# Optimization experiments

Measured on AMD Instinct MI355X. Metric: run time of the kernel, lower is better.

The kernel has to match this reference:

```python
import jax, jax.numpy as jnp
import numpy as np

N = 50000
E = 800000
D = 64  # d_s


def _mlp2(x, w1, b1, w2, b2):
    # Linear -> SiLU -> Linear
    return jax.nn.silu(x @ w1 + b1) @ w2 + b2


def setup_inputs() -> dict:
    key = jax.random.key(0)
    ks = jax.random.split(key, 20)
    s = jax.random.normal(ks[0], (N, D), jnp.float32)
    v = jax.random.normal(ks[1], (N, 3), jnp.float32)
    edge_index = jax.random.randint(ks[2], (2, E), 0, N, jnp.int32)
    edge_attr = jax.random.normal(ks[3], (E, D), jnp.float32)
    ev = jax.random.normal(ks[4], (E, 3), jnp.float32)
    edge_vec_unit = ev / jnp.linalg.norm(ev, axis=-1, keepdims=True)

    def lin(k, fan_in, fan_out):
        kw, kb = jax.random.split(k)
        lim = 1.0 / np.sqrt(fan_in)
        w = jax.random.uniform(kw, (fan_in, fan_out), jnp.float32, -lim, lim)
        b = jax.random.uniform(kb, (fan_out,), jnp.float32, -lim, lim)
        return w, b

    ng_w1, ng_b1 = lin(ks[5], D + 1, D)
    ng_w2, ng_b2 = lin(ks[6], D, D)
    eg_w1, eg_b1 = lin(ks[7], D + 1, D)
    eg_w2, eg_b2 = lin(ks[8], D, D)
    mg_w1, mg_b1 = lin(ks[9], 3 * D, 2 * D)
    mg_w2, mg_b2 = lin(ks[10], 2 * D, D)
    pe_w, pe_b = lin(ks[11], D, 1)
    up_w, up_b = lin(ks[12], D, D)
    ln_g = jnp.ones((D,), jnp.float32)
    ln_b = jnp.zeros((D,), jnp.float32)
    return dict(s=s, v=v, edge_index=edge_index, edge_attr=edge_attr,
                edge_vec_unit=edge_vec_unit,
                ng_w1=ng_w1, ng_b1=ng_b1, ng_w2=ng_w2, ng_b2=ng_b2,
                eg_w1=eg_w1, eg_b1=eg_b1, eg_w2=eg_w2, eg_b2=eg_b2,
                mg_w1=mg_w1, mg_b1=mg_b1, mg_w2=mg_w2, mg_b2=mg_b2,
                pe_w=pe_w, pe_b=pe_b, up_w=up_w, up_b=up_b,
                ln_g=ln_g, ln_b=ln_b)


def reference(s, v, edge_index, edge_attr, edge_vec_unit,
              ng_w1, ng_b1, ng_w2, ng_b2,
              eg_w1, eg_b1, eg_w2, eg_b2,
              mg_w1, mg_b1, mg_w2, mg_b2,
              pe_w, pe_b, up_w, up_b, ln_g, ln_b):
    row, col = edge_index[0], edge_index[1]
    s_i, s_j = s[row], s[col]            # (E, D)
    v_i, v_j = v[row], v[col]            # (E, 3)

    dot_ij = jnp.sum(v_i * edge_vec_unit, axis=-1, keepdims=True)
    dot_ji = jnp.sum(v_j * -edge_vec_unit, axis=-1, keepdims=True)
    res_ij = 1.0 - dot_ij
    res_ji = 1.0 - dot_ji
    cross_mag = jnp.linalg.norm(jnp.cross(v_i, v_j), axis=-1, keepdims=True)

    node_feat_i = _mlp2(jnp.concatenate([s_i, res_ij], -1), ng_w1, ng_b1, ng_w2, ng_b2)
    node_feat_j = _mlp2(jnp.concatenate([s_j, res_ji], -1), ng_w1, ng_b1, ng_w2, ng_b2)
    edge_feat = _mlp2(jnp.concatenate([edge_attr, cross_mag], -1), eg_w1, eg_b1, eg_w2, eg_b2)

    msg = _mlp2(jnp.concatenate([node_feat_i, node_feat_j, edge_feat], -1),
                mg_w1, mg_b1, mg_w2, mg_b2)   # (E, D)
    coeff = msg @ pe_w + pe_b                 # (E, 1)
    v_msg = edge_vec_unit * coeff             # (E, 3)

    n = s.shape[0]
    s_agg = jax.ops.segment_sum(msg, row, num_segments=n)    # (N, D)
    v_agg = jax.ops.segment_sum(v_msg, row, num_segments=n)  # (N, 3)

    s_new = s + jax.nn.silu(s_agg) @ up_w + up_b
    mu = jnp.mean(s_new, axis=-1, keepdims=True)
    var = jnp.var(s_new, axis=-1, keepdims=True)
    s_out = (s_new - mu) * jax.lax.rsqrt(var + 1e-5) * ln_g + ln_b

    v_new = v + v_agg
    denom = jnp.maximum(jnp.linalg.norm(v_new, axis=-1, keepdims=True), 1e-6)
    v_out = v_new / denom
    return (s_out, v_out)
```

## Files before the change

### kernel.cpp

```cpp
#include <hip/hip_runtime.h>
#include <math.h>

#define NN 50000
#define NE 800000
#define D 64

typedef __attribute__((ext_vector_type(8))) short short8;
typedef __attribute__((ext_vector_type(4))) float f32x4;

__device__ __forceinline__ float silu_f(float x) { return x / (1.0f + __expf(-x)); }
__device__ __forceinline__ unsigned short f2bf(float f) {
  unsigned int u = __float_as_uint(f);
  u += 0x7fffu + ((u >> 16) & 1u);
  return (unsigned short)(u >> 16);
}
__device__ __forceinline__ unsigned int pack2(float a, float b) {
  return (unsigned int)f2bf(a) | ((unsigned int)f2bf(b) << 16);
}
__device__ __forceinline__ short8 pack_frag(f32x4 a, f32x4 b) {
  union { unsigned int u[4]; short8 s; } r;
  r.u[0] = pack2(a[0], a[1]);
  r.u[1] = pack2(a[2], a[3]);
  r.u[2] = pack2(b[0], b[1]);
  r.u[3] = pack2(b[2], b[3]);
  return r.s;
}

__global__ void prep_all(const float* __restrict__ ng_w2,
                         const float* __restrict__ eg_w1,
                         const float* __restrict__ eg_w2,
                         const float* __restrict__ mg_w1,
                         const float* __restrict__ mg_w2,
                         const float* __restrict__ ng_w1,
                         const float* __restrict__ up_w,
                         unsigned short* __restrict__ out) {
  int t = blockIdx.x * 256 + threadIdx.x;
  if (t >= 104 * 64) return;
  int frag = t >> 6, L = t & 63;
  const float* W; int K, N, f0;
  if (frag < 8)       { W = ng_w2; K = 64;  N = 64;  f0 = 0; }
  else if (frag < 16) { W = eg_w1; K = 64;  N = 64;  f0 = 8; }
  else if (frag < 24) { W = eg_w2; K = 64;  N = 64;  f0 = 16; }
  else if (frag < 72) { W = mg_w1; K = 192; N = 128; f0 = 24; }
  else if (frag < 88) { W = mg_w2; K = 128; N = 64;  f0 = 72; }
  else if (frag < 96) { W = ng_w1; K = 64;  N = 64;  f0 = 88; }
  else                { W = up_w;  K = 64;  N = 64;  f0 = 96; }
  int lf = frag - f0;
  int kd = K >> 5;
  int nt = lf / kd, ks = lf % kd;
  int kb = ks * 32 + (L >> 4) * 8;
  int nc = nt * 16 + (L & 15);
  unsigned int p[4];
#pragma unroll
  for (int jj = 0; jj < 4; ++jj) {
    float a = W[(size_t)(kb + 2 * jj) * N + nc];
    float b = W[(size_t)(kb + 2 * jj + 1) * N + nc];
    p[jj] = pack2(a, b);
  }
  *(uint4*)(out + (size_t)frag * 512 + L * 8) = make_uint4(p[0], p[1], p[2], p[3]);
}

__global__ __launch_bounds__(256, 4) void node_pre(
    const float* __restrict__ s, const float* __restrict__ ng_b1,
    const unsigned short* __restrict__ WF, float* __restrict__ h_ng) {
  __shared__ __align__(16) char sm[4 * 8704];
  int tid = threadIdx.x, w = tid >> 6, lane = tid & 63;
  int l15 = lane & 15, q = lane >> 4, fb = q * 8;
  char* my = sm + w * 8704;
  int nb = (blockIdx.x * 4 + w) * 32;
  if (nb >= NN) return;

  short8 Bs[2][2];
#pragma unroll
  for (int h = 0; h < 2; ++h)
#pragma unroll
    for (int kt = 0; kt < 2; ++kt) {
      int n = nb + h * 16 + l15; if (n >= NN) n = NN - 1;
      f32x4 x0 = *(const f32x4*)(s + (size_t)n * D + kt * 32 + fb);
      f32x4 x1 = *(const f32x4*)(s + (size_t)n * D + kt * 32 + fb + 4);
      Bs[h][kt] = pack_frag(x0, x1);
    }
  short8 F[4][2]; f32x4 bb[4];
#pragma unroll
  for (int mt = 0; mt < 4; ++mt) {
    F[mt][0] = *(const short8*)(WF + (size_t)(88 + mt * 2 + 0) * 512 + lane * 8);
    F[mt][1] = *(const short8*)(WF + (size_t)(88 + mt * 2 + 1) * 512 + lane * 8);
    bb[mt] = *(const f32x4*)(ng_b1 + mt * 16 + 4 * q);
  }
#pragma unroll
  for (int h = 0; h < 2; ++h)
#pragma unroll
    for (int mt = 0; mt < 4; ++mt) {
      f32x4 acc = {0.f, 0.f, 0.f, 0.f};
      acc = __builtin_amdgcn_mfma_f32_16x16x32_bf16(F[mt][0], Bs[h][0], acc, 0, 0, 0);
      acc = __builtin_amdgcn_mfma_f32_16x16x32_bf16(F[mt][1], Bs[h][1], acc, 0, 0, 0);
      acc[0] += bb[mt][0]; acc[1] += bb[mt][1]; acc[2] += bb[mt][2]; acc[3] += bb[mt][3];
      *(f32x4*)(my + (((h * 16 + l15) * 68 + mt * 16 + 4 * q) << 2)) = acc;
    }
#pragma unroll
  for (int h = 0; h < 2; ++h)
#pragma unroll
    for (int e = 0; e < 16; ++e) {
      int n = nb + h * 16 + e;
      if (n < NN) {
        float val = *(const float*)(my + (((h * 16 + e) * 68 + lane) << 2));
        h_ng[(size_t)n * D + lane] = val;
      }
    }
}

#define LSTR 104
#define LDSW (32 * LSTR * 4)

__global__ __launch_bounds__(256, 3) void edge_mfma(
    const float* __restrict__ v, const int* __restrict__ ei,
    const float* __restrict__ edge_attr, const float* __restrict__ evu,
    const float* __restrict__ ng_w1, const float* __restrict__ ng_b2,
    const float* __restrict__ eg_w1, const float* __restrict__ eg_b1,
    const float* __restrict__ eg_b2,
    const float* __restrict__ mg_b1, const float* __restrict__ mg_b2,
    const float* __restrict__ pe_w, const float* __restrict__ pe_b,
    const float* __restrict__ h_ng,
    const unsigned short* __restrict__ WF,
    float* __restrict__ s_agg, float* __restrict__ v_agg) {
  __shared__ __align__(16) char sm[4 * LDSW];
  int tid = threadIdx.x, w = tid >> 6, lane = tid & 63;
  int l15 = lane & 15, q = lane >> 4, fb = q * 8;
  char* my = sm + w * LDSW;
  int eb = (blockIdx.x * 4 + w) * 32;

  int rown[2], coln[2];
  float rij[2], rji[2], uu0[2], uu1[2], uu2[2], cmag[2];
#pragma unroll
  for (int h = 0; h < 2; ++h) {
    int e = eb + h * 16 + l15;
    int r = ei[e], c = ei[NE + e];
    rown[h] = r; coln[h] = c;
    float u0 = evu[e * 3 + 0], u1 = evu[e * 3 + 1], u2 = evu[e * 3 + 2];
    uu0[h] = u0; uu1[h] = u1; uu2[h] = u2;
    float vi0 = v[r * 3 + 0], vi1 = v[r * 3 + 1], vi2 = v[r * 3 + 2];
    float vj0 = v[c * 3 + 0], vj1 = v[c * 3 + 1], vj2 = v[c * 3 + 2];
    rij[h] = 1.f - (vi0 * u0 + vi1 * u1 + vi2 * u2);
    rji[h] = 1.f + (vj0 * u0 + vj1 * u1 + vj2 * u2);
    float cx = vi1 * vj2 - vi2 * vj1;
    float cy = vi2 * vj0 - vi0 * vj2;
    float cz = vi0 * vj1 - vi1 * vj0;
    cmag[h] = sqrtf(cx * cx + cy * cy + cz * cz);
  }

  short8 Bai[2][2], Baj[2][2], Bxe[2][2];
  f32x4 w1l[2][2];
#pragma unroll
  for (int kt = 0; kt < 2; ++kt) {
    w1l[kt][0] = *(const f32x4*)(ng_w1 + 64 * 64 + kt * 32 + fb);
    w1l[kt][1] = *(const f32x4*)(ng_w1 + 64 * 64 + kt * 32 + fb + 4);
  }
#pragma unroll
  for (int h = 0; h < 2; ++h)
#pragma unroll
    for (int kt = 0; kt < 2; ++kt) {
      const float* pr = h_ng + (size_t)rown[h] * D + kt * 32 + fb;
      const float* pc = h_ng + (size_t)coln[h] * D + kt * 32 + fb;
      const float* px = edge_attr + (size_t)(eb + h * 16 + l15) * D + kt * 32 + fb;
      f32x4 a0 = *(const f32x4*)pr, a1 = *(const f32x4*)(pr + 4);
      f32x4 b0 = *(const f32x4*)pc, b1 = *(const f32x4*)(pc + 4);
      f32x4 x0 = *(const f32x4*)px, x1 = *(const f32x4*)(px + 4);
      f32x4 si0, si1, sj0, sj1;
#pragma unroll
      for (int c2 = 0; c2 < 4; ++c2) {
        si0[c2] = silu_f(a0[c2] + rij[h] * w1l[kt][0][c2]);
        si1[c2] = silu_f(a1[c2] + rij[h] * w1l[kt][1][c2]);
        sj0[c2] = silu_f(b0[c2] + rji[h] * w1l[kt][0][c2]);
        sj1[c2] = silu_f(b1[c2] + rji[h] * w1l[kt][1][c2]);
      }
      Bai[h][kt] = pack_frag(si0, si1);
      Baj[h][kt] = pack_frag(sj0, sj1);
      Bxe[h][kt] = pack_frag(x0, x1);
    }

  {
    short8 F[4][2]; f32x4 bb[4];
#pragma unroll
    for (int mt = 0; mt < 4; ++mt) {
      F[mt][0] = *(const short8*)(WF + (size_t)(0 + mt * 2 + 0) * 512 + lane * 8);
      F[mt][1] = *(const short8*)(WF + (size_t)(0 + mt * 2 + 1) * 512 + lane * 8);
      bb[mt] = *(const f32x4*)(ng_b2 + mt * 16 + 4 * q);
    }
#pragma unroll
    for (int h = 0; h < 2; ++h)
#pragma unroll
      for (int mt = 0; mt < 4; ++mt) {
        f32x4 ai = {0.f, 0.f, 0.f, 0.f}, aj = {0.f, 0.f, 0.f, 0.f};
        ai = __builtin_amdgcn_mfma_f32_16x16x32_bf16(F[mt][0], Bai[h][0], ai, 0, 0, 0);
        ai = __builtin_amdgcn_mfma_f32_16x16x32_bf16(F[mt][1], Bai[h][1], ai, 0, 0, 0);
        aj = __builtin_amdgcn_mfma_f32_16x16x32_bf16(F[mt][0], Baj[h][0], aj, 0, 0, 0);
        aj = __builtin_amdgcn_mfma_f32_16x16x32_bf16(F[mt][1], Baj[h][1], aj, 0, 0, 0);
        uint2 pi, pj;
        pi.x = pack2(ai[0] + bb[mt][0], ai[1] + bb[mt][1]);
        pi.y = pack2(ai[2] + bb[mt][2], ai[3] + bb[mt][3]);
        pj.x = pack2(aj[0] + bb[mt][0], aj[1] + bb[mt][1]);
        pj.y = pack2(aj[2] + bb[mt][2], aj[3] + bb[mt][3]);
        int row = h * 16 + l15;
        *(uint2*)(my + ((row * LSTR + mt * 8 + 2 * q) << 2)) = pi;
        *(uint2*)(my + ((row * LSTR + 32 + mt * 8 + 2 * q) << 2)) = pj;
      }
  }

  {
    short8 F[4][2]; f32x4 bb[4], el[4];
#pragma unroll
    for (int mt = 0; mt < 4; ++mt) {
      F[mt][0] = *(const short8*)(WF + (size_t)(8 + mt * 2 + 0) * 512 + lane * 8);
      F[mt][1] = *(const short8*)(WF + (size_t)(8 + mt * 2 + 1) * 512 + lane * 8);
      bb[mt] = *(const f32x4*)(eg_b1 + mt * 16 + 4 * q);
      el[mt] = *(const f32x4*)(eg_w1 + 64 * 64 + mt * 16 + 4 * q);
    }
#pragma unroll
    for (int h = 0; h < 2; ++h)
#pragma unroll
      for (int mt = 0; mt < 4; ++mt) {
        f32x4 acc = {0.f, 0.f, 0.f, 0.f};
        acc = __builtin_amdgcn_mfma_f32_16x16x32_bf16(F[mt][0], Bxe[h][0], acc, 0, 0, 0);
        acc = __builtin_amdgcn_mfma_f32_16x16x32_bf16(F[mt][1], Bxe[h][1], acc, 0, 0, 0);
        float t0 = silu_f(acc[0] + bb[mt][0] + cmag[h] * el[mt][0]);
        float t1 = silu_f(acc[1] + bb[mt][1] + cmag[h] * el[mt][1]);
        float t2 = silu_f(acc[2] + bb[mt][2] + cmag[h] * el[mt][2]);
        float t3 = silu_f(acc[3] + bb[mt][3] + cmag[h] * el[mt][3]);
        uint2 p; p.x = pack2(t0, t1); p.y = pack2(t2, t3);
        *(uint2*)(my + (((h * 16 + l15) * LSTR + 64 + mt * 8 + 2 * q) << 2)) = p;
      }
  }

  {
    short8 Bae[2][2];
#pragma unroll
    for (int h = 0; h < 2; ++h)
#pragma unroll
      for (int kt = 0; kt < 2; ++kt)
        Bae[h][kt] = *(const short8*)(my + (((h * 16 + l15) * LSTR + 64 + 16 * kt + 4 * q) << 2));
    short8 F[4][2]; f32x4 bb[4];
#pragma unroll
    for (int mt = 0; mt < 4; ++mt) {
      F[mt][0] = *(const short8*)(WF + (size_t)(16 + mt * 2 + 0) * 512 + lane * 8);
      F[mt][1] = *(const short8*)(WF + (size_t)(16 + mt * 2 + 1) * 512 + lane * 8);
      bb[mt] = *(const f32x4*)(eg_b2 + mt * 16 + 4 * q);
    }
#pragma unroll
    for (int h = 0; h < 2; ++h)
#pragma unroll
      for (int mt = 0; mt < 4; ++mt) {
        f32x4 acc = {0.f, 0.f, 0.f, 0.f};
        acc = __builtin_amdgcn_mfma_f32_16x16x32_bf16(F[mt][0], Bae[h][0], acc, 0, 0, 0);
        acc = __builtin_amdgcn_mfma_f32_16x16x32_bf16(F[mt][1], Bae[h][1], acc, 0, 0, 0);
        uint2 p;
        p.x = pack2(acc[0] + bb[mt][0], acc[1] + bb[mt][1]);
        p.y = pack2(acc[2] + bb[mt][2], acc[3] + bb[mt][3]);
        *(uint2*)(my + (((h * 16 + l15) * LSTR + 64 + mt * 8 + 2 * q) << 2)) = p;
      }
  }

  {
    short8 Bin[2][6];
#pragma unroll
    for (int h = 0; h < 2; ++h)
#pragma unroll
      for (int kt = 0; kt < 6; ++kt)
        Bin[h][kt] = *(const short8*)(my + (((h * 16 + l15) * LSTR + 16 * kt + 4 * q) << 2));
#pragma unroll
    for (int mt = 0; mt < 8; ++mt) {
      short8 F[6];
#pragma unroll
      for (int ks = 0; ks < 6; ++ks)
        F[ks] = *(const short8*)(WF + (size_t)(24 + mt * 6 + ks) * 512 + lane * 8);
      f32x4 bb = *(const f32x4*)(mg_b1 + mt * 16 + 4 * q);
#pragma unroll
      for (int h = 0; h < 2; ++h) {
        f32x4 acc = {0.f, 0.f, 0.f, 0.f};
#pragma unroll
        for (int ks = 0; ks < 6; ++ks)
          acc = __builtin_amdgcn_mfma_f32_16x16x32_bf16(F[ks], Bin[h][ks], acc, 0, 0, 0);
        uint2 p;
        p.x = pack2(silu_f(acc[0] + bb[0]), silu_f(acc[1] + bb[1]));
        p.y = pack2(silu_f(acc[2] + bb[2]), silu_f(acc[3] + bb[3]));
        *(uint2*)(my + (((h * 16 + l15) * LSTR + mt * 8 + 2 * q) << 2)) = p;
      }
    }
  }

  f32x4 msg[2][4];
  {
    short8 Bh[2][4];
#pragma unroll
    for (int h = 0; h < 2; ++h)
#pragma unroll
      for (int kt = 0; kt < 4; ++kt)
        Bh[h][kt] = *(const short8*)(my + (((h * 16 + l15) * LSTR + 16 * kt + 4 * q) << 2));
#pragma unroll
    for (int mt = 0; mt < 4; ++mt) {
      short8 F[4];
#pragma unroll
      for (int ks = 0; ks < 4; ++ks)
        F[ks] = *(const short8*)(WF + (size_t)(72 + mt * 4 + ks) * 512 + lane * 8);
      f32x4 bb = *(const f32x4*)(mg_b2 + mt * 16 + 4 * q);
#pragma unroll
      for (int h = 0; h < 2; ++h) {
        f32x4 acc = {0.f, 0.f, 0.f, 0.f};
#pragma unroll
        for (int ks = 0; ks < 4; ++ks)
          acc = __builtin_amdgcn_mfma_f32_16x16x32_bf16(F[ks], Bh[h][ks], acc, 0, 0, 0);
        acc[0] += bb[0]; acc[1] += bb[1]; acc[2] += bb[2]; acc[3] += bb[3];
        msg[h][mt] = acc;
      }
    }
  }

  float part[2] = {0.f, 0.f};
#pragma unroll
  for (int mt = 0; mt < 4; ++mt) {
    f32x4 pw4 = *(const f32x4*)(pe_w + mt * 16 + 4 * q);
#pragma unroll
    for (int h = 0; h < 2; ++h)
      part[h] += msg[h][mt][0] * pw4[0] + msg[h][mt][1] * pw4[1] +
                 msg[h][mt][2] * pw4[2] + msg[h][mt][3] * pw4[3];
  }
  float peb = pe_b[0];
#pragma unroll
  for (int h = 0; h < 2; ++h) {
    part[h] += __shfl_xor(part[h], 16, 64);
    part[h] += __shfl_xor(part[h], 32, 64);
    if (q < 3) {
      float uc = (q == 0) ? uu0[h] : ((q == 1) ? uu1[h] : uu2[h]);
      atomicAdd(&v_agg[(size_t)rown[h] * 3 + q], uc * (part[h] + peb));
    }
  }

#pragma unroll
  for (int h = 0; h < 2; ++h)
#pragma unroll
    for (int mt = 0; mt < 4; ++mt)
      *(f32x4*)(my + (((h * 16 + l15) * LSTR + mt * 16 + 4 * q) << 2)) = msg[h][mt];
#pragma unroll
  for (int h = 0; h < 2; ++h)
#pragma unroll
    for (int e = 0; e < 16; ++e) {
      int sr = __builtin_amdgcn_readlane(rown[h], e);
      float val = *(const float*)(my + (((h * 16 + e) * LSTR + lane) << 2));
      atomicAdd(&s_agg[(size_t)sr * D + lane], val);
    }
}

__global__ __launch_bounds__(256, 4) void node_out(
    const float* __restrict__ s, const float* __restrict__ v,
    const float* __restrict__ up_b,
    const float* __restrict__ ln_g, const float* __restrict__ ln_b,
    const float* __restrict__ s_agg, const float* __restrict__ v_agg,
    const unsigned short* __restrict__ WF, float* __restrict__ out) {
  __shared__ __align__(16) char sm[4 * 8704];
  int tid = threadIdx.x, w = tid >> 6, lane = tid & 63;
  int l15 = lane & 15, q = lane >> 4, fb = q * 8;
  char* my = sm + w * 8704;
  int nb = (blockIdx.x * 4 + w) * 32;
  if (nb >= NN) return;

  short8 Bg[2][2];
#pragma unroll
  for (int h = 0; h < 2; ++h)
#pragma unroll
    for (int kt = 0; kt < 2; ++kt) {
      int n = nb + h * 16 + l15; if (n >= NN) n = NN - 1;
      f32x4 g0 = *(const f32x4*)(s_agg + (size_t)n * D + kt * 32 + fb);
      f32x4 g1 = *(const f32x4*)(s_agg + (size_t)n * D + kt * 32 + fb + 4);
#pragma unroll
      for (int c2 = 0; c2 < 4; ++c2) { g0[c2] = silu_f(g0[c2]); g1[c2] = silu_f(g1[c2]); }
      Bg[h][kt] = pack_frag(g0, g1);
    }
  short8 F[4][2]; f32x4 bb[4];
#pragma unroll
  for (int mt = 0; mt < 4; ++mt) {
    F[mt][0] = *(const short8*)(WF + (size_t)(96 + mt * 2 + 0) * 512 + lane * 8);
    F[mt][1] = *(const short8*)(WF + (size_t)(96 + mt * 2 + 1) * 512 + lane * 8);
    bb[mt] = *(const f32x4*)(up_b + mt * 16 + 4 * q);
  }
  f32x4 sn[2][4];
#pragma unroll
  for (int h = 0; h < 2; ++h) {
    int n = nb + h * 16 + l15; if (n >= NN) n = NN - 1;
#pragma unroll
    for (int mt = 0; mt < 4; ++mt) {
      f32x4 acc = {0.f, 0.f, 0.f, 0.f};
      acc = __builtin_amdgcn_mfma_f32_16x16x32_bf16(F[mt][0], Bg[h][0], acc, 0, 0, 0);
      acc = __builtin_amdgcn_mfma_f32_16x16x32_bf16(F[mt][1], Bg[h][1], acc, 0, 0, 0);
      f32x4 sv = *(const f32x4*)(s + (size_t)n * D + mt * 16 + 4 * q);
      sn[h][mt][0] = acc[0] + bb[mt][0] + sv[0];
      sn[h][mt][1] = acc[1] + bb[mt][1] + sv[1];
      sn[h][mt][2] = acc[2] + bb[mt][2] + sv[2];
      sn[h][mt][3] = acc[3] + bb[mt][3] + sv[3];
    }
  }
#pragma unroll
  for (int h = 0; h < 2; ++h) {
    float m = 0.f;
#pragma unroll
    for (int mt = 0; mt < 4; ++mt)
      m += sn[h][mt][0] + sn[h][mt][1] + sn[h][mt][2] + sn[h][mt][3];
    m += __shfl_xor(m, 16, 64);
    m += __shfl_xor(m, 32, 64);
    float mu = m * (1.f / 64.f);
    float vv = 0.f;
#pragma unroll
    for (int mt = 0; mt < 4; ++mt)
#pragma unroll
      for (int r = 0; r < 4; ++r) {
        float d = sn[h][mt][r] - mu;
        vv += d * d;
      }
    vv += __shfl_xor(vv, 16, 64);
    vv += __shfl_xor(vv, 32, 64);
    float inv = 1.f / sqrtf(vv * (1.f / 64.f) + 1e-5f);
#pragma unroll
    for (int mt = 0; mt < 4; ++mt) {
      f32x4 lg = *(const f32x4*)(ln_g + mt * 16 + 4 * q);
      f32x4 lb = *(const f32x4*)(ln_b + mt * 16 + 4 * q);
      f32x4 ov;
#pragma unroll
      for (int r = 0; r < 4; ++r) ov[r] = (sn[h][mt][r] - mu) * inv * lg[r] + lb[r];
      *(f32x4*)(my + (((h * 16 + l15) * 68 + mt * 16 + 4 * q) << 2)) = ov;
    }
  }
#pragma unroll
  for (int h = 0; h < 2; ++h)
#pragma unroll
    for (int e = 0; e < 16; ++e) {
      int n = nb + h * 16 + e;
      if (n < NN) {
        float val = *(const float*)(my + (((h * 16 + e) * 68 + lane) << 2));
        out[(size_t)n * D + lane] = val;
      }
    }
#pragma unroll
  for (int h = 0; h < 2; ++h) {
    int n = nb + h * 16 + l15;
    if (q < 3 && n < NN) {
      float v0 = v[n * 3 + 0] + v_agg[(size_t)n * 3 + 0];
      float v1 = v[n * 3 + 1] + v_agg[(size_t)n * 3 + 1];
      float v2 = v[n * 3 + 2] + v_agg[(size_t)n * 3 + 2];
      float nrm = sqrtf(v0 * v0 + v1 * v1 + v2 * v2);
      float denom = fmaxf(nrm, 1e-6f);
      float val = (q == 0) ? v0 : ((q == 1) ? v1 : v2);
      out[(size_t)NN * D + (size_t)n * 3 + q] = val / denom;
    }
  }
}

extern "C" void kernel_launch(void* const* d_in, const int* in_sizes, int n_in,
                              void* d_out, int out_size, void* d_ws, size_t ws_size,
                              hipStream_t stream) {
  const float* s         = (const float*)d_in[0];
  const float* v         = (const float*)d_in[1];
  const int*   ei        = (const int*)d_in[2];
  const float* edge_attr = (const float*)d_in[3];
  const float* evu       = (const float*)d_in[4];
  const float* ng_w1     = (const float*)d_in[5];
  const float* ng_b1     = (const float*)d_in[6];
  const float* ng_w2     = (const float*)d_in[7];
  const float* ng_b2     = (const float*)d_in[8];
  const float* eg_w1     = (const float*)d_in[9];
  const float* eg_b1     = (const float*)d_in[10];
  const float* eg_w2     = (const float*)d_in[11];
  const float* eg_b2     = (const float*)d_in[12];
  const float* mg_w1     = (const float*)d_in[13];
  const float* mg_b1     = (const float*)d_in[14];
  const float* mg_w2     = (const float*)d_in[15];
  const float* mg_b2     = (const float*)d_in[16];
  const float* pe_w      = (const float*)d_in[17];
  const float* pe_b      = (const float*)d_in[18];
  const float* up_w      = (const float*)d_in[19];
  const float* up_b      = (const float*)d_in[20];
  const float* ln_g      = (const float*)d_in[21];
  const float* ln_b      = (const float*)d_in[22];
  (void)in_sizes; (void)n_in; (void)out_size; (void)ws_size;

  float* out   = (float*)d_out;
  float* s_agg = (float*)d_ws;
  float* v_agg = s_agg + (size_t)NN * D;
  unsigned short* WF = (unsigned short*)(v_agg + (size_t)NN * 3);
  float* h_ng  = out;

  hipMemsetAsync(d_ws, 0, (size_t)(NN * D + NN * 3) * sizeof(float), stream);

  prep_all<<<26, 256, 0, stream>>>(ng_w2, eg_w1, eg_w2, mg_w1, mg_w2, ng_w1, up_w, WF);

  int node_blocks = (NN + 127) / 128;
  node_pre<<<node_blocks, 256, 0, stream>>>(s, ng_b1, WF, h_ng);

  edge_mfma<<<NE / 128, 256, 0, stream>>>(
      v, ei, edge_attr, evu,
      ng_w1, ng_b2, eg_w1, eg_b1, eg_b2,
      mg_b1, mg_b2, pe_w, pe_b, h_ng, WF, s_agg, v_agg);

  node_out<<<node_blocks, 256, 0, stream>>>(
      s, v, up_b, ln_g, ln_b, s_agg, v_agg, WF, out);
}
```

Measured before the change: 587.3 us.

## Shrink per-wave LDS staging to double-buffered half tiles for higher occupancy

```diff
diff --git a/kernel.cpp b/kernel.cpp
--- a/kernel.cpp
+++ b/kernel.cpp
@@ -7,6 +7,8 @@
 
 typedef __attribute__((ext_vector_type(8))) short short8;
 typedef __attribute__((ext_vector_type(4))) float f32x4;
+
+__device__ __forceinline__ void lds_fence() { asm volatile("" ::: "memory"); }
 
 __device__ __forceinline__ float silu_f(float x) { return x / (1.0f + __expf(-x)); }
 __device__ __forceinline__ unsigned short f2bf(float f) {
@@ -97,6 +99,7 @@
       acc[0] += bb[mt][0]; acc[1] += bb[mt][1]; acc[2] += bb[mt][2]; acc[3] += bb[mt][3];
       *(f32x4*)(my + (((h * 16 + l15) * 68 + mt * 16 + 4 * q) << 2)) = acc;
     }
+  lds_fence();
 #pragma unroll
   for (int h = 0; h < 2; ++h)
 #pragma unroll
@@ -109,10 +112,23 @@
     }
 }
 
-#define LSTR 104
-#define LDSW (32 * LSTR * 4)
-
-__global__ __launch_bounds__(256, 3) void edge_mfma(
+#define TB 2304
+#define WSLICE (2 * TB)
+
+__device__ __forceinline__ void put_tile(char* buf, int l15, int q, int mtl,
+                                         int h, unsigned int px, unsigned int py) {
+  *(uint2*)(buf + (((h * 16 + l15) * 18 + mtl * 8 + 2 * q) << 2)) = make_uint2(px, py);
+}
+__device__ __forceinline__ short8 get_frag(const char* buf, int l15, int q, int h) {
+  const char* p = buf + (((h * 16 + l15) * 18 + 4 * q) << 2);
+  uint2 lo = *(const uint2*)p;
+  uint2 hi = *(const uint2*)(p + 8);
+  union { unsigned int u[4]; short8 s; } r;
+  r.u[0] = lo.x; r.u[1] = lo.y; r.u[2] = hi.x; r.u[3] = hi.y;
+  return r.s;
+}
+
+__global__ __launch_bounds__(256, 4) void edge_mfma(
     const float* __restrict__ v, const int* __restrict__ ei,
     const float* __restrict__ edge_attr, const float* __restrict__ evu,
     const float* __restrict__ ng_w1, const float* __restrict__ ng_b2,
@@ -123,10 +139,10 @@
     const float* __restrict__ h_ng,
     const unsigned short* __restrict__ WF,
     float* __restrict__ s_agg, float* __restrict__ v_agg) {
-  __shared__ __align__(16) char sm[4 * LDSW];
+  __shared__ __align__(16) char sm[4 * WSLICE];
   int tid = threadIdx.x, w = tid >> 6, lane = tid & 63;
   int l15 = lane & 15, q = lane >> 4, fb = q * 8;
-  char* my = sm + w * LDSW;
+  char* my = sm + w * WSLICE;
   int eb = (blockIdx.x * 4 + w) * 32;
 
   int rown[2], coln[2];
@@ -148,37 +164,37 @@
     cmag[h] = sqrtf(cx * cx + cy * cy + cz * cz);
   }
 
-  short8 Bai[2][2], Baj[2][2], Bxe[2][2];
   f32x4 w1l[2][2];
 #pragma unroll
   for (int kt = 0; kt < 2; ++kt) {
     w1l[kt][0] = *(const f32x4*)(ng_w1 + 64 * 64 + kt * 32 + fb);
     w1l[kt][1] = *(const f32x4*)(ng_w1 + 64 * 64 + kt * 32 + fb + 4);
   }
-#pragma unroll
-  for (int h = 0; h < 2; ++h)
-#pragma unroll
-    for (int kt = 0; kt < 2; ++kt) {
-      const float* pr = h_ng + (size_t)rown[h] * D + kt * 32 + fb;
-      const float* pc = h_ng + (size_t)coln[h] * D + kt * 32 + fb;
-      const float* px = edge_attr + (size_t)(eb + h * 16 + l15) * D + kt * 32 + fb;
-      f32x4 a0 = *(const f32x4*)pr, a1 = *(const f32x4*)(pr + 4);
-      f32x4 b0 = *(const f32x4*)pc, b1 = *(const f32x4*)(pc + 4);
-      f32x4 x0 = *(const f32x4*)px, x1 = *(const f32x4*)(px + 4);
-      f32x4 si0, si1, sj0, sj1;
-#pragma unroll
-      for (int c2 = 0; c2 < 4; ++c2) {
-        si0[c2] = silu_f(a0[c2] + rij[h] * w1l[kt][0][c2]);
-        si1[c2] = silu_f(a1[c2] + rij[h] * w1l[kt][1][c2]);
-        sj0[c2] = silu_f(b0[c2] + rji[h] * w1l[kt][0][c2]);
-        sj1[c2] = silu_f(b1[c2] + rji[h] * w1l[kt][1][c2]);
-      }
-      Bai[h][kt] = pack_frag(si0, si1);
-      Baj[h][kt] = pack_frag(sj0, sj1);
-      Bxe[h][kt] = pack_frag(x0, x1);
-    }
+
+  short8 Bin[2][6];
 
   {
+    short8 Bai[2][2], Baj[2][2];
+#pragma unroll
+    for (int h = 0; h < 2; ++h)
+#pragma unroll
+      for (int kt = 0; kt < 2; ++kt) {
+        const float* pr = h_ng + (size_t)rown[h] * D + kt * 32 + fb;
+        const float* pc = h_ng + (size_t)coln[h] * D + kt * 32 + fb;
+        f32x4 a0 = *(const f32x4*)pr, a1 = *(const f32x4*)(pr + 4);
+        f32x4 b0 = *(const f32x4*)pc, b1 = *(const f32x4*)(pc + 4);
+        f32x4 si0, si1, sj0, sj1;
+#pragma unroll
+        for (int c2 = 0; c2 < 4; ++c2) {
+          si0[c2] = silu_f(a0[c2] + rij[h] * w1l[kt][0][c2]);
+          si1[c2] = silu_f(a1[c2] + rij[h] * w1l[kt][1][c2]);
+          sj0[c2] = silu_f(b0[c2] + rji[h] * w1l[kt][0][c2]);
+          sj1[c2] = silu_f(b1[c2] + rji[h] * w1l[kt][1][c2]);
+        }
+        Bai[h][kt] = pack_frag(si0, si1);
+        Baj[h][kt] = pack_frag(sj0, sj1);
+      }
+
     short8 F[4][2]; f32x4 bb[4];
 #pragma unroll
     for (int mt = 0; mt < 4; ++mt) {
@@ -187,87 +203,132 @@
       bb[mt] = *(const f32x4*)(ng_b2 + mt * 16 + 4 * q);
     }
 #pragma unroll
+    for (int kt = 0; kt < 2; ++kt) {
+      char* buf = my + kt * TB;
+#pragma unroll
+      for (int mtl = 0; mtl < 2; ++mtl) {
+        int mt = kt * 2 + mtl;
+#pragma unroll
+        for (int h = 0; h < 2; ++h) {
+          f32x4 acc = {0.f, 0.f, 0.f, 0.f};
+          acc = __builtin_amdgcn_mfma_f32_16x16x32_bf16(F[mt][0], Bai[h][0], acc, 0, 0, 0);
+          acc = __builtin_amdgcn_mfma_f32_16x16x32_bf16(F[mt][1], Bai[h][1], acc, 0, 0, 0);
+          put_tile(buf, l15, q, mtl, h,
+                   pack2(acc[0] + bb[mt][0], acc[1] + bb[mt][1]),
+                   pack2(acc[2] + bb[mt][2], acc[3] + bb[mt][3]));
+        }
+      }
+      lds_fence();
+#pragma unroll
+      for (int h = 0; h < 2; ++h) Bin[h][kt] = get_frag(buf, l15, q, h);
+      lds_fence();
+    }
+#pragma unroll
+    for (int kt = 0; kt < 2; ++kt) {
+      char* buf = my + kt * TB;
+#pragma unroll
+      for (int mtl = 0; mtl < 2; ++mtl) {
+        int mt = kt * 2 + mtl;
+#pragma unroll
+        for (int h = 0; h < 2; ++h) {
+          f32x4 acc = {0.f, 0.f, 0.f, 0.f};
+          acc = __builtin_amdgcn_mfma_f32_16x16x32_bf16(F[mt][0], Baj[h][0], acc, 0, 0, 0);
+          acc = __builtin_amdgcn_mfma_f32_16x16x32_bf16(F[mt][1], Baj[h][1], acc, 0, 0, 0);
+          put_tile(buf, l15, q, mtl, h,
+                   pack2(acc[0] + bb[mt][0], acc[1] + bb[mt][1]),
+                   pack2(acc[2] + bb[mt][2], acc[3] + bb[mt][3]));
+        }
+      }
+      lds_fence();
+#pragma unroll
+      for (int h = 0; h < 2; ++h) Bin[h][2 + kt] = get_frag(buf, l15, q, h);
+      lds_fence();
+    }
+  }
+
+  {
+    short8 Bxe[2][2];
+#pragma unroll
     for (int h = 0; h < 2; ++h)
 #pragma unroll
+      for (int kt = 0; kt < 2; ++kt) {
+        const float* px = edge_attr + (size_t)(eb + h * 16 + l15) * D + kt * 32 + fb;
+        f32x4 x0 = *(const f32x4*)px, x1 = *(const f32x4*)(px + 4);
+        Bxe[h][kt] = pack_frag(x0, x1);
+      }
+    short8 Bae[2][2];
+    {
+      short8 F[4][2]; f32x4 bb[4], el[4];
+#pragma unroll
       for (int mt = 0; mt < 4; ++mt) {
-        f32x4 ai = {0.f, 0.f, 0.f, 0.f}, aj = {0.f, 0.f, 0.f, 0.f};
-        ai = __builtin_amdgcn_mfma_f32_16x16x32_bf16(F[mt][0], Bai[h][0], ai, 0, 0, 0);
-        ai = __builtin_amdgcn_mfma_f32_16x16x32_bf16(F[mt][1], Bai[h][1], ai, 0, 0, 0);
-        aj = __builtin_amdgcn_mfma_f32_16x16x32_bf16(F[mt][0], Baj[h][0], aj, 0, 0, 0);
-        aj = __builtin_amdgcn_mfma_f32_16x16x32_bf16(F[mt][1], Baj[h][1], aj, 0, 0, 0);
-        uint2 pi, pj;
-        pi.x = pack2(ai[0] + bb[mt][0], ai[1] + bb[mt][1]);
-        pi.y = pack2(ai[2] + bb[mt][2], ai[3] + bb[mt][3]);
-        pj.x = pack2(aj[0] + bb[mt][0], aj[1] + bb[mt][1]);
-        pj.y = pack2(aj[2] + bb[mt][2], aj[3] + bb[mt][3]);
-        int row = h * 16 + l15;
-        *(uint2*)(my + ((row * LSTR + mt * 8 + 2 * q) << 2)) = pi;
-        *(uint2*)(my + ((row * LSTR + 32 + mt * 8 + 2 * q) << 2)) = pj;
-      }
-  }
-
-  {
-    short8 F[4][2]; f32x4 bb[4], el[4];
-#pragma unroll
-    for (int mt = 0; mt < 4; ++mt) {
-      F[mt][0] = *(const short8*)(WF + (size_t)(8 + mt * 2 + 0) * 512 + lane * 8);
-      F[mt][1] = *(const short8*)(WF + (size_t)(8 + mt * 2 + 1) * 512 + lane * 8);
-      bb[mt] = *(const f32x4*)(eg_b1 + mt * 16 + 4 * q);
-      el[mt] = *(const f32x4*)(eg_w1 + 64 * 64 + mt * 16 + 4 * q);
-    }
-#pragma unroll
-    for (int h = 0; h < 2; ++h)
+        F[mt][0] = *(const short8*)(WF + (size_t)(8 + mt * 2 + 0) * 512 + lane * 8);
+        F[mt][1] = *(const short8*)(WF + (size_t)(8 + mt * 2 + 1) * 512 + lane * 8);
+        bb[mt] = *(const f32x4*)(eg_b1 + mt * 16 + 4 * q);
+        el[mt] = *(const f32x4*)(eg_w1 + 64 * 64 + mt * 16 + 4 * q);
+      }
+#pragma unroll
+      for (int kt = 0; kt < 2; ++kt) {
+        char* buf = my + kt * TB;
+#pragma unroll
+        for (int mtl = 0; mtl < 2; ++mtl) {
+          int mt = kt * 2 + mtl;
+#pragma unroll
+          for (int h = 0; h < 2; ++h) {
+            f32x4 acc = {0.f, 0.f, 0.f, 0.f};
+            acc = __builtin_amdgcn_mfma_f32_16x16x32_bf16(F[mt][0], Bxe[h][0], acc, 0, 0, 0);
+            acc = __builtin_amdgcn_mfma_f32_16x16x32_bf16(F[mt][1], Bxe[h][1], acc, 0, 0, 0);
+            float t0 = silu_f(acc[0] + bb[mt][0] + cmag[h] * el[mt][0]);
+            float t1 = silu_f(acc[1] + bb[mt][1] + cmag[h] * el[mt][1]);
+            float t2 = silu_f(acc[2] + bb[mt][2] + cmag[h] * el[mt][2]);
+            float t3 = silu_f(acc[3] + bb[mt][3] + cmag[h] * el[mt][3]);
+            put_tile(buf, l15, q, mtl, h, pack2(t0, t1), pack2(t2, t3));
+          }
+        }
+        lds_fence();
+#pragma unroll
+        for (int h = 0; h < 2; ++h) Bae[h][kt] = get_frag(buf, l15, q, h);
+        lds_fence();
+      }
+    }
+    {
+      short8 F[4][2]; f32x4 bb[4];
 #pragma unroll
       for (int mt = 0; mt < 4; ++mt) {
-        f32x4 acc = {0.f, 0.f, 0.f, 0.f};
-        acc = __builtin_amdgcn_mfma_f32_16x16x32_bf16(F[mt][0], Bxe[h][0], acc, 0, 0, 0);
-        acc = __builtin_amdgcn_mfma_f32_16x16x32_bf16(F[mt][1], Bxe[h][1], acc, 0, 0, 0);
-        float t0 = silu_f(acc[0] + bb[mt][0] + cmag[h] * el[mt][0]);
-        float t1 = silu_f(acc[1] + bb[mt][1] + cmag[h] * el[mt][1]);
-        float t2 = silu_f(acc[2] + bb[mt][2] + cmag[h] * el[mt][2]);
-        float t3 = silu_f(acc[3] + bb[mt][3] + cmag[h] * el[mt][3]);
-        uint2 p; p.x = pack2(t0, t1); p.y = pack2(t2, t3);
-        *(uint2*)(my + (((h * 16 + l15) * LSTR + 64 + mt * 8 + 2 * q) << 2)) = p;
-      }
-  }
-
-  {
-    short8 Bae[2][2];
-#pragma unroll
-    for (int h = 0; h < 2; ++h)
-#pragma unroll
-      for (int kt = 0; kt < 2; ++kt)
-        Bae[h][kt] = *(const short8*)(my + (((h * 16 + l15) * LSTR + 64 + 16 * kt + 4 * q) << 2));
-    short8 F[4][2]; f32x4 bb[4];
-#pragma unroll
-    for (int mt = 0; mt < 4; ++mt) {
-      F[mt][0] = *(const short8*)(WF + (size_t)(16 + mt * 2 + 0) * 512 + lane * 8);
-      F[mt][1] = *(const short8*)(WF + (size_t)(16 + mt * 2 + 1) * 512 + lane * 8);
-      bb[mt] = *(const f32x4*)(eg_b2 + mt * 16 + 4 * q);
-    }
-#pragma unroll
-    for (int h = 0; h < 2; ++h)
-#pragma unroll
-      for (int mt = 0; mt < 4; ++mt) {
-        f32x4 acc = {0.f, 0.f, 0.f, 0.f};
-        acc = __builtin_amdgcn_mfma_f32_16x16x32_bf16(F[mt][0], Bae[h][0], acc, 0, 0, 0);
-        acc = __builtin_amdgcn_mfma_f32_16x16x32_bf16(F[mt][1], Bae[h][1], acc, 0, 0, 0);
-        uint2 p;
-        p.x = pack2(acc[0] + bb[mt][0], acc[1] + bb[mt][1]);
-        p.y = pack2(acc[2] + bb[mt][2], acc[3] + bb[mt][3]);
-        *(uint2*)(my + (((h * 16 + l15) * LSTR + 64 + mt * 8 + 2 * q) << 2)) = p;
-      }
-  }
-
-  {
-    short8 Bin[2][6];
-#pragma unroll
-    for (int h = 0; h < 2; ++h)
-#pragma unroll
-      for (int kt = 0; kt < 6; ++kt)
-        Bin[h][kt] = *(const short8*)(my + (((h * 16 + l15) * LSTR + 16 * kt + 4 * q) << 2));
-#pragma unroll
-    for (int mt = 0; mt < 8; ++mt) {
+        F[mt][0] = *(const short8*)(WF + (size_t)(16 + mt * 2 + 0) * 512 + lane * 8);
+        F[mt][1] = *(const short8*)(WF + (size_t)(16 + mt * 2 + 1) * 512 + lane * 8);
+        bb[mt] = *(const f32x4*)(eg_b2 + mt * 16 + 4 * q);
+      }
+#pragma unroll
+      for (int kt = 0; kt < 2; ++kt) {
+        char* buf = my + kt * TB;
+#pragma unroll
+        for (int mtl = 0; mtl < 2; ++mtl) {
+          int mt = kt * 2 + mtl;
+#pragma unroll
+          for (int h = 0; h < 2; ++h) {
+            f32x4 acc = {0.f, 0.f, 0.f, 0.f};
+            acc = __builtin_amdgcn_mfma_f32_16x16x32_bf16(F[mt][0], Bae[h][0], acc, 0, 0, 0);
+            acc = __builtin_amdgcn_mfma_f32_16x16x32_bf16(F[mt][1], Bae[h][1], acc, 0, 0, 0);
+            put_tile(buf, l15, q, mtl, h,
+                     pack2(acc[0] + bb[mt][0], acc[1] + bb[mt][1]),
+                     pack2(acc[2] + bb[mt][2], acc[3] + bb[mt][3]));
+          }
+        }
+        lds_fence();
+#pragma unroll
+        for (int h = 0; h < 2; ++h) Bin[h][4 + kt] = get_frag(buf, l15, q, h);
+        lds_fence();
+      }
+    }
+  }
+
+  short8 Bh[2][4];
+#pragma unroll
+  for (int kt = 0; kt < 4; ++kt) {
+    char* buf = my + (kt & 1) * TB;
+#pragma unroll
+    for (int mtl = 0; mtl < 2; ++mtl) {
+      int mt = kt * 2 + mtl;
       short8 F[6];
 #pragma unroll
       for (int ks = 0; ks < 6; ++ks)
@@ -279,38 +340,33 @@
 #pragma unroll
         for (int ks = 0; ks < 6; ++ks)
           acc = __builtin_amdgcn_mfma_f32_16x16x32_bf16(F[ks], Bin[h][ks], acc, 0, 0, 0);
-        uint2 p;
-        p.x = pack2(silu_f(acc[0] + bb[0]), silu_f(acc[1] + bb[1]));
-        p.y = pack2(silu_f(acc[2] + bb[2]), silu_f(acc[3] + bb[3]));
-        *(uint2*)(my + (((h * 16 + l15) * LSTR + mt * 8 + 2 * q) << 2)) = p;
-      }
-    }
+        put_tile(buf, l15, q, mtl, h,
+                 pack2(silu_f(acc[0] + bb[0]), silu_f(acc[1] + bb[1])),
+                 pack2(silu_f(acc[2] + bb[2]), silu_f(acc[3] + bb[3])));
+      }
+    }
+    lds_fence();
+#pragma unroll
+    for (int h = 0; h < 2; ++h) Bh[h][kt] = get_frag(buf, l15, q, h);
+    lds_fence();
   }
 
   f32x4 msg[2][4];
-  {
-    short8 Bh[2][4];
-#pragma unroll
-    for (int h = 0; h < 2; ++h)
-#pragma unroll
-      for (int kt = 0; kt < 4; ++kt)
-        Bh[h][kt] = *(const short8*)(my + (((h * 16 + l15) * LSTR + 16 * kt + 4 * q) << 2));
-#pragma unroll
-    for (int mt = 0; mt < 4; ++mt) {
-      short8 F[4];
+#pragma unroll
+  for (int mt = 0; mt < 4; ++mt) {
+    short8 F[4];
+#pragma unroll
+    for (int ks = 0; ks < 4; ++ks)
+      F[ks] = *(const short8*)(WF + (size_t)(72 + mt * 4 + ks) * 512 + lane * 8);
+    f32x4 bb = *(const f32x4*)(mg_b2 + mt * 16 + 4 * q);
+#pragma unroll
+    for (int h = 0; h < 2; ++h) {
+      f32x4 acc = {0.f, 0.f, 0.f, 0.f};
 #pragma unroll
       for (int ks = 0; ks < 4; ++ks)
-        F[ks] = *(const short8*)(WF + (size_t)(72 + mt * 4 + ks) * 512 + lane * 8);
-      f32x4 bb = *(const f32x4*)(mg_b2 + mt * 16 + 4 * q);
-#pragma unroll
-      for (int h = 0; h < 2; ++h) {
-        f32x4 acc = {0.f, 0.f, 0.f, 0.f};
-#pragma unroll
-        for (int ks = 0; ks < 4; ++ks)
-          acc = __builtin_amdgcn_mfma_f32_16x16x32_bf16(F[ks], Bh[h][ks], acc, 0, 0, 0);
-        acc[0] += bb[0]; acc[1] += bb[1]; acc[2] += bb[2]; acc[3] += bb[3];
-        msg[h][mt] = acc;
-      }
+        acc = __builtin_amdgcn_mfma_f32_16x16x32_bf16(F[ks], Bh[h][ks], acc, 0, 0, 0);
+      acc[0] += bb[0]; acc[1] += bb[1]; acc[2] += bb[2]; acc[3] += bb[3];
+      msg[h][mt] = acc;
     }
   }
 
@@ -337,15 +393,20 @@
 #pragma unroll
   for (int h = 0; h < 2; ++h)
 #pragma unroll
-    for (int mt = 0; mt < 4; ++mt)
-      *(f32x4*)(my + (((h * 16 + l15) * LSTR + mt * 16 + 4 * q) << 2)) = msg[h][mt];
-#pragma unroll
-  for (int h = 0; h < 2; ++h)
-#pragma unroll
-    for (int e = 0; e < 16; ++e) {
-      int sr = __builtin_amdgcn_readlane(rown[h], e);
-      float val = *(const float*)(my + (((h * 16 + e) * LSTR + lane) << 2));
-      atomicAdd(&s_agg[(size_t)sr * D + lane], val);
+    for (int c = 0; c < 2; ++c) {
+      if ((l15 >> 3) == c) {
+#pragma unroll
+        for (int mt = 0; mt < 4; ++mt)
+          *(f32x4*)(my + (((l15 & 7) * 68 + mt * 16 + 4 * q) << 2)) = msg[h][mt];
+      }
+      lds_fence();
+#pragma unroll
+      for (int e = 0; e < 8; ++e) {
+        int sr = __builtin_amdgcn_readlane(rown[h], c * 8 + e);
+        float val = *(const float*)(my + ((e * 68 + lane) << 2));
+        atomicAdd(&s_agg[(size_t)sr * D + lane], val);
+      }
+      lds_fence();
     }
 }
 
@@ -427,6 +488,7 @@
       *(f32x4*)(my + (((h * 16 + l15) * 68 + mt * 16 + 4 * q) << 2)) = ov;
     }
   }
+  lds_fence();
 #pragma unroll
   for (int h = 0; h < 2; ++h)
 #pragma unroll
```

Result: slower. 663.7 us (+13.0%).
